# Kernel optimization log

Measured on AMD Instinct MI355X. Metric: run time of the kernel, lower is better.

Reference implementation:

```python
import jax, jax.numpy as jnp
import numpy as np

N_NODES = 100000
IN_DIM = 64
EMB_DIM = 128
N_EDGES = 1600000
BN_EPS = 1e-5
GIN_EPS = 0.0  # train_eps=False, default eps=0


def setup_inputs() -> dict:
    key = jax.random.key(0)
    ks = jax.random.split(key, 10)
    x = jax.random.normal(ks[0], (N_NODES, IN_DIM), dtype=jnp.float32)
    edge_index = jax.random.randint(ks[1], (2, N_EDGES), 0, N_NODES, dtype=jnp.int64)
    edge_attr = jax.random.normal(ks[2], (N_EDGES, 4), dtype=jnp.float32)  # unused by module
    edge_weight = jax.random.uniform(ks[3], (N_EDGES,), dtype=jnp.float32)
    # MLP params: Linear(in,emb) -> BN(emb) -> ReLU -> Linear(emb,emb)
    lim1 = 1.0 / np.sqrt(IN_DIM)
    W1 = jax.random.uniform(ks[4], (IN_DIM, EMB_DIM), minval=-lim1, maxval=lim1, dtype=jnp.float32)
    b1 = jax.random.uniform(ks[5], (EMB_DIM,), minval=-lim1, maxval=lim1, dtype=jnp.float32)
    gamma = jnp.ones((EMB_DIM,), dtype=jnp.float32)
    beta = jnp.zeros((EMB_DIM,), dtype=jnp.float32)
    lim2 = 1.0 / np.sqrt(EMB_DIM)
    W2 = jax.random.uniform(ks[6], (EMB_DIM, EMB_DIM), minval=-lim2, maxval=lim2, dtype=jnp.float32)
    b2 = jax.random.uniform(ks[7], (EMB_DIM,), minval=-lim2, maxval=lim2, dtype=jnp.float32)
    return {"x": x, "edge_index": edge_index, "edge_attr": edge_attr,
            "edge_weight": edge_weight, "W1": W1, "b1": b1,
            "gamma": gamma, "beta": beta, "W2": W2, "b2": b2}


def reference(x, edge_index, edge_attr, edge_weight, W1, b1, gamma, beta, W2, b2):
    src, dst = edge_index[0], edge_index[1]  # message from x[src] aggregated at dst
    msg = x[src] * edge_weight[:, None]                       # [E, in_dim] gather + scale
    agg = jax.ops.segment_sum(msg, dst, num_segments=x.shape[0])  # [N, in_dim] scatter-add
    out = agg + (1.0 + GIN_EPS) * x                           # GIN self term
    # MLP: Linear -> BatchNorm1d (training stats, biased var) -> ReLU -> Linear
    h = out @ W1 + b1                                         # [N, emb]
    mean = jnp.mean(h, axis=0)
    var = jnp.var(h, axis=0)
    h = (h - mean) * jax.lax.rsqrt(var + BN_EPS) * gamma + beta
    h = jax.nn.relu(h)
    return h @ W2 + b2
```

## Files before the change

### kernel.cpp

```cpp
#include <hip/hip_runtime.h>

#define N_NODES 100000
#define IN_DIM 64
#define EMB 128
#define N_EDGES 1600000
#define BN_EPS 1e-5f

#define NB 98
#define BCAP 18432
#define FA_THREADS 512
#define FA_EPT 16
#define FA_BLK (FA_THREADS * FA_EPT)
#define FA_GRID ((N_EDGES + FA_BLK - 1) / FA_BLK)

#define WS_GSUM     0
#define WS_GSUM2    512
#define WS_BCUR     1024
#define WS_ROWSTART 2048
#define WS_PAIRS    802304
#define WS_AGG      13602304
#define WS_DSTARR   39202304
#define WS_SWARR    46427648
#define WS_X16      WS_DSTARR
#define WS_ZERO_INTS 512

typedef _Float16 half8_t __attribute__((ext_vector_type(8)));
typedef _Float16 half4_t __attribute__((ext_vector_type(4)));
typedef _Float16 half2_t __attribute__((ext_vector_type(2)));
typedef float floatx4 __attribute__((ext_vector_type(4)));

__global__ __launch_bounds__(512) void zero_kernel(int* __restrict__ p)
{
    p[threadIdx.x] = 0;
}

__global__ __launch_bounds__(512) void fillA_kernel(
    const int* __restrict__ ei, const float* __restrict__ ew,
    int* __restrict__ bcur, int* __restrict__ dstArr, float2* __restrict__ swArr)
{
    __shared__ int cnt[NB], base[NB];
    const int tid = threadIdx.x;
    if (tid < NB) cnt[tid] = 0;
    __syncthreads();
    const int e0 = blockIdx.x * FA_BLK;
    int pk[FA_EPT];
    #pragma unroll
    for (int i = 0; i < FA_EPT; ++i) {
        int e = e0 + i * FA_THREADS + tid;
        pk[i] = -1;
        if (e < N_EDGES) {
            int d = ei[N_EDGES + e];
            int b = d >> 10;
            int pos = atomicAdd(&cnt[b], 1);
            pk[i] = (b << 13) | pos;
        }
    }
    __syncthreads();
    if (tid < NB) base[tid] = atomicAdd(&bcur[tid], cnt[tid]);
    __syncthreads();
    #pragma unroll
    for (int i = 0; i < FA_EPT; ++i) {
        int e = e0 + i * FA_THREADS + tid;
        if (pk[i] >= 0) {
            int b = pk[i] >> 13, pos = pk[i] & 8191;
            int idx = b * BCAP + base[b] + pos;
            dstArr[idx] = ei[N_EDGES + e];
            swArr[idx]  = make_float2(__int_as_float(ei[e]), ew[e]);
        }
    }
}

__global__ __launch_bounds__(1024) void fillB2_kernel(
    const int* __restrict__ bcur, const int* __restrict__ dstArr,
    const float2* __restrict__ swArr,
    int* __restrict__ rowstart, float2* __restrict__ pairs)
{
    __shared__ int cnt2[1024];
    __shared__ int pre[1024];
    __shared__ int sbk[128];
    const int g = blockIdx.x;
    const int tid = threadIdx.x;

    if (tid < 128) sbk[tid] = (tid < NB) ? bcur[tid] : 0;
    cnt2[tid] = 0;
    __syncthreads();
    for (int off = 1; off < 128; off <<= 1) {
        int v = 0;
        if (tid < 128 && tid >= off) v = sbk[tid - off];
        __syncthreads();
        if (tid < 128) sbk[tid] += v;
        __syncthreads();
    }
    const int bucketBase = (g > 0) ? sbk[g - 1] : 0;

    const int nE = bcur[g];
    const int segBase = g * BCAP;
    for (int j = tid; j < nE; j += 1024)
        atomicAdd(&cnt2[dstArr[segBase + j] & 1023], 1);
    __syncthreads();

    const int c = cnt2[tid];
    pre[tid] = c;
    __syncthreads();
    for (int off = 1; off < 1024; off <<= 1) {
        int v = (tid >= off) ? pre[tid - off] : 0;
        __syncthreads();
        pre[tid] += v;
        __syncthreads();
    }
    const int start = bucketBase + pre[tid] - c;
    const int node = g * 1024 + tid;
    if (node < N_NODES) rowstart[node] = start;
    if (node == N_NODES - 1) rowstart[N_NODES] = start + c;

    __syncthreads();
    cnt2[tid] = start;
    __syncthreads();
    #pragma unroll 4
    for (int j = tid; j < nE; j += 1024) {
        int d = dstArr[segBase + j];
        int p = atomicAdd(&cnt2[d & 1023], 1);
        pairs[p] = swArr[segBase + j];
    }
}

__global__ __launch_bounds__(256) void cvt_kernel(
    const float4* __restrict__ x4, ushort4* __restrict__ x16)
{
    int i = blockIdx.x * 256 + threadIdx.x;
    if (i >= N_NODES * IN_DIM / 4) return;
    float4 v = x4[i];
    ushort4 u;
    _Float16 a = (_Float16)v.x, b = (_Float16)v.y,
             c = (_Float16)v.z, d = (_Float16)v.w;
    u.x = *(unsigned short*)&a; u.y = *(unsigned short*)&b;
    u.z = *(unsigned short*)&c; u.w = *(unsigned short*)&d;
    x16[i] = u;
}

#define G_NPW 5
__global__ __launch_bounds__(256) void gather_kernel(
    const _Float16* __restrict__ x16,
    const int* __restrict__ rowstart,
    const float2* __restrict__ pairs,
    float* __restrict__ agg)
{
    const int tid  = threadIdx.x;
    const int lane = tid & 63;
    const int wid  = tid >> 6;
    const int e    = lane >> 4;
    const int f    = lane & 15;
    const half4_t* __restrict__ xv4 = (const half4_t*)x16;
    const int node0 = (blockIdx.x * 4 + wid) * G_NPW;

    for (int r = 0; r < G_NPW; ++r) {
        const int n  = node0 + r;
        const int jb = rowstart[n];
        const int je = rowstart[n + 1];
        float4 accA = make_float4(0.f, 0.f, 0.f, 0.f);
        float4 accB = make_float4(0.f, 0.f, 0.f, 0.f);
        for (int j0 = jb; j0 < je; j0 += 64) {
            const int cnt = min(64, je - j0);
            float2 p = (lane < cnt) ? pairs[j0 + lane] : make_float2(0.f, 0.f);
            int   psrc = __float_as_int(p.x);
            float pw   = p.y;
            const int nch = (cnt + 7) >> 3;
            #pragma unroll 4
            for (int c = 0; c < nch; ++c) {
                int   uA = __shfl(psrc, c * 8 + e);
                float wA = __shfl(pw,   c * 8 + e);
                int   uB = __shfl(psrc, c * 8 + 4 + e);
                float wB = __shfl(pw,   c * 8 + 4 + e);
                half4_t va = xv4[(size_t)(unsigned)uA * 16 + f];
                half4_t vb = xv4[(size_t)(unsigned)uB * 16 + f];
                accA.x += wA * (float)va[0]; accA.y += wA * (float)va[1];
                accA.z += wA * (float)va[2]; accA.w += wA * (float)va[3];
                accB.x += wB * (float)vb[0]; accB.y += wB * (float)vb[1];
                accB.z += wB * (float)vb[2]; accB.w += wB * (float)vb[3];
            }
        }
        float4 s = make_float4(accA.x + accB.x, accA.y + accB.y,
                               accA.z + accB.z, accA.w + accB.w);
        s.x += __shfl_xor(s.x, 16); s.y += __shfl_xor(s.y, 16);
        s.z += __shfl_xor(s.z, 16); s.w += __shfl_xor(s.w, 16);
        s.x += __shfl_xor(s.x, 32); s.y += __shfl_xor(s.y, 32);
        s.z += __shfl_xor(s.z, 32); s.w += __shfl_xor(s.w, 32);
        if (e == 0)
            *(float4*)&agg[(size_t)n * IN_DIM + f * 4] = s;
    }
}

#define GV_TPW 3
#define GV_TILES (N_NODES / 16)
#define GV_GRID ((GV_TILES + 4 * GV_TPW - 1) / (4 * GV_TPW))
__global__ __launch_bounds__(256) void gemv_kernel(
    const float* __restrict__ agg,
    const float* __restrict__ x,
    const float* __restrict__ W1,
    const float* __restrict__ b1,
    _Float16* __restrict__ h16,
    float* __restrict__ gsum, float* __restrict__ gsum2)
{
    __shared__ _Float16 w1t[EMB][72];
    __shared__ float redS[4][EMB], redQ[4][EMB];

    const int tid  = threadIdx.x;
    const int lane = tid & 63;
    const int wid  = tid >> 6;
    const int l15  = lane & 15;
    const int kb   = lane >> 4;

    #pragma unroll
    for (int i = 0; i < 32; ++i) {
        int idx = i * 256 + tid;
        int k = idx >> 7, c = idx & 127;
        w1t[c][k] = (_Float16)W1[idx];
    }
    float b1c[8];
    #pragma unroll
    for (int ct = 0; ct < 8; ++ct) b1c[ct] = b1[ct * 16 + l15];
    __syncthreads();

    half8_t Bf[8][2];
    #pragma unroll
    for (int ct = 0; ct < 8; ++ct)
        #pragma unroll
        for (int kc = 0; kc < 2; ++kc)
            Bf[ct][kc] = *(half8_t*)&w1t[ct * 16 + l15][kc * 32 + kb * 8];

    float sA[8] = {0,0,0,0,0,0,0,0};
    float qA[8] = {0,0,0,0,0,0,0,0};

    #pragma unroll
    for (int j = 0; j < GV_TPW; ++j) {
        const int t = blockIdx.x * (4 * GV_TPW) + wid * GV_TPW + j;
        if (t >= GV_TILES) break;
        const size_t rowb = (size_t)(t * 16 + l15) * IN_DIM + kb * 8;
        half8_t af[2];
        #pragma unroll
        for (int kc = 0; kc < 2; ++kc) {
            float4 a0 = *(const float4*)(agg + rowb + kc * 32);
            float4 a1 = *(const float4*)(agg + rowb + kc * 32 + 4);
            float4 x0 = *(const float4*)(x   + rowb + kc * 32);
            float4 x1 = *(const float4*)(x   + rowb + kc * 32 + 4);
            af[kc][0] = (_Float16)(a0.x + x0.x);
            af[kc][1] = (_Float16)(a0.y + x0.y);
            af[kc][2] = (_Float16)(a0.z + x0.z);
            af[kc][3] = (_Float16)(a0.w + x0.w);
            af[kc][4] = (_Float16)(a1.x + x1.x);
            af[kc][5] = (_Float16)(a1.y + x1.y);
            af[kc][6] = (_Float16)(a1.z + x1.z);
            af[kc][7] = (_Float16)(a1.w + x1.w);
        }
        floatx4 acc[8];
        #pragma unroll
        for (int ct = 0; ct < 8; ++ct)
            acc[ct] = (floatx4){b1c[ct], b1c[ct], b1c[ct], b1c[ct]};
        #pragma unroll
        for (int kc = 0; kc < 2; ++kc)
            #pragma unroll
            for (int ct = 0; ct < 8; ++ct)
                acc[ct] = __builtin_amdgcn_mfma_f32_16x16x32_f16(af[kc], Bf[ct][kc], acc[ct], 0, 0, 0);
        #pragma unroll
        for (int ct = 0; ct < 8; ++ct) {
            #pragma unroll
            for (int i = 0; i < 4; ++i) {
                const int r = t * 16 + kb * 4 + i;
                const float v = acc[ct][i];
                h16[(size_t)r * EMB + ct * 16 + l15] = (_Float16)v;
                sA[ct] += v;
                qA[ct] += v * v;
            }
        }
    }

    #pragma unroll
    for (int ct = 0; ct < 8; ++ct) {
        sA[ct] += __shfl_xor(sA[ct], 16); sA[ct] += __shfl_xor(sA[ct], 32);
        qA[ct] += __shfl_xor(qA[ct], 16); qA[ct] += __shfl_xor(qA[ct], 32);
    }
    if (lane < 16) {
        #pragma unroll
        for (int ct = 0; ct < 8; ++ct) {
            redS[wid][ct * 16 + lane] = sA[ct];
            redQ[wid][ct * 16 + lane] = qA[ct];
        }
    }
    __syncthreads();
    if (tid < EMB) {
        float s = redS[0][tid] + redS[1][tid] + redS[2][tid] + redS[3][tid];
        float q = redQ[0][tid] + redQ[1][tid] + redQ[2][tid] + redQ[3][tid];
        atomicAdd(&gsum[tid],  s);
        atomicAdd(&gsum2[tid], q);
    }
}

#define MR 32
#define M2_ITERS 5
#define M2_ROWS (MR * M2_ITERS)

__global__ __launch_bounds__(256) void mlp2_kernel(
    const _Float16* __restrict__ h16,
    float* __restrict__ out,
    const float* __restrict__ gsum, const float* __restrict__ gsum2,
    const float* __restrict__ gamma, const float* __restrict__ beta,
    const float* __restrict__ W2,
    const float* __restrict__ b2)
{
    __shared__ _Float16 Ph[MR][136];
    __shared__ float abuf[EMB], bbuf[EMB];

    const int tid  = threadIdx.x;
    const int lane = tid & 63;
    const int wid  = tid >> 6;
    const int rg   = wid >> 1;
    const int ch   = wid & 1;
    const int c0w  = ch * 64;
    const int l15  = lane & 15;
    const int kb   = lane >> 4;

    if (tid < EMB) {
        const float invN = 1.0f / (float)N_NODES;
        float mean = gsum[tid] * invN;
        float var  = gsum2[tid] * invN - mean * mean;
        float inv  = rsqrtf(var + BN_EPS);
        float a    = gamma[tid] * inv;
        abuf[tid] = a;
        bbuf[tid] = beta[tid] - mean * a;
    }

    const int bcol = c0w + l15;
    half8_t Bf[4][4];
    #pragma unroll
    for (int ct = 0; ct < 4; ++ct) {
        #pragma unroll
        for (int kc = 0; kc < 4; ++kc) {
            #pragma unroll
            for (int i = 0; i < 8; ++i)
                Bf[ct][kc][i] = (_Float16)W2[(kc * 32 + kb * 8 + i) * EMB + ct * 16 + bcol];
        }
    }
    float b2c[4];
    #pragma unroll
    for (int ct = 0; ct < 4; ++ct) b2c[ct] = b2[ct * 16 + bcol];

    __syncthreads();

    const int r0blk = blockIdx.x * M2_ROWS;
    for (int it = 0; it < M2_ITERS; ++it) {
        const int r0 = r0blk + it * MR;
        #pragma unroll
        for (int i = 0; i < 8; ++i) {
            int j   = i * 256 + tid;
            int row = j >> 6;
            int c2  = (j & 63) * 2;
            half2_t hv = *(const half2_t*)&h16[(size_t)(r0 + row) * EMB + c2];
            float p0 = fmaxf((float)hv[0] * abuf[c2]     + bbuf[c2],     0.f);
            float p1 = fmaxf((float)hv[1] * abuf[c2 + 1] + bbuf[c2 + 1], 0.f);
            Ph[row][c2]     = (_Float16)p0;
            Ph[row][c2 + 1] = (_Float16)p1;
        }
        __syncthreads();

        floatx4 acc[4];
        #pragma unroll
        for (int ct = 0; ct < 4; ++ct)
            acc[ct] = (floatx4){b2c[ct], b2c[ct], b2c[ct], b2c[ct]};
        #pragma unroll
        for (int kc = 0; kc < 4; ++kc) {
            half8_t af = *(half8_t*)&Ph[rg * 16 + l15][kc * 32 + kb * 8];
            #pragma unroll
            for (int ct = 0; ct < 4; ++ct)
                acc[ct] = __builtin_amdgcn_mfma_f32_16x16x32_f16(af, Bf[ct][kc], acc[ct], 0, 0, 0);
        }
        __syncthreads();

        #pragma unroll
        for (int ct = 0; ct < 4; ++ct) {
            #pragma unroll
            for (int i = 0; i < 4; ++i) {
                int row = r0 + rg * 16 + kb * 4 + i;
                out[(size_t)row * EMB + c0w + ct * 16 + l15] = acc[ct][i];
            }
        }
    }
}

extern "C" void kernel_launch(void* const* d_in, const int* in_sizes, int n_in,
                              void* d_out, int out_size, void* d_ws, size_t ws_size,
                              hipStream_t stream)
{
    const float* x     = (const float*)d_in[0];
    const int*   ei    = (const int*)d_in[1];
    const float* ew    = (const float*)d_in[3];
    const float* W1    = (const float*)d_in[4];
    const float* b1    = (const float*)d_in[5];
    const float* gamma = (const float*)d_in[6];
    const float* beta  = (const float*)d_in[7];
    const float* W2    = (const float*)d_in[8];
    const float* b2    = (const float*)d_in[9];

    char* ws = (char*)d_ws;
    float*    gsum     = (float*)(ws + WS_GSUM);
    float*    gsum2    = (float*)(ws + WS_GSUM2);
    int*      bcur     = (int*)(ws + WS_BCUR);
    int*      rowstart = (int*)(ws + WS_ROWSTART);
    float2*   pairs    = (float2*)(ws + WS_PAIRS);
    float*    agg      = (float*)(ws + WS_AGG);
    _Float16* h16      = (_Float16*)(ws + WS_AGG);
    int*      dstArr   = (int*)(ws + WS_DSTARR);
    float2*   swArr    = (float2*)(ws + WS_SWARR);
    _Float16* x16      = (_Float16*)(ws + WS_X16);
    float*    out      = (float*)d_out;

    zero_kernel<<<1, WS_ZERO_INTS, 0, stream>>>((int*)d_ws);
    fillA_kernel<<<FA_GRID, FA_THREADS, 0, stream>>>(ei, ew, bcur, dstArr, swArr);
    fillB2_kernel<<<NB, 1024, 0, stream>>>(bcur, dstArr, swArr, rowstart, pairs);
    cvt_kernel<<<(N_NODES * IN_DIM / 4 + 255) / 256, 256, 0, stream>>>(
        (const float4*)x, (ushort4*)x16);
    gather_kernel<<<N_NODES / (4 * G_NPW), 256, 0, stream>>>(x16, rowstart, pairs, agg);
    gemv_kernel<<<GV_GRID, 256, 0, stream>>>(agg, x, W1, b1, h16, gsum, gsum2);
    mlp2_kernel<<<N_NODES / M2_ROWS, 256, 0, stream>>>(h16, out, gsum, gsum2, gamma, beta, W2, b2);
}
```

Measured before the change: 156.6 us.

## Fuse neighbor gather with first linear layer and BN statistics

Merges the gather/aggregate kernel and the first MFMA GEMM kernel into one. Each block aggregates 32 nodes into a shared-memory fp16 tile, adding the self term from the fp16 copy of x, then runs the 64x128 product and BN partial sums from that tile. This removes the fp32 agg round trip through global memory and one launch. In exchange, every block reloads and converts W1 into shared memory, and the self term now uses fp16 x instead of fp32 x.

```diff
diff --git a/kernel.cpp b/kernel.cpp
--- a/kernel.cpp
+++ b/kernel.cpp
@@ -18,7 +18,7 @@
 #define WS_BCUR     1024
 #define WS_ROWSTART 2048
 #define WS_PAIRS    802304
-#define WS_AGG      13602304
+#define WS_H16      13602304
 #define WS_DSTARR   39202304
 #define WS_SWARR    46427648
 #define WS_X16      WS_DSTARR
@@ -138,23 +138,43 @@
     x16[i] = u;
 }
 
-#define G_NPW 5
-__global__ __launch_bounds__(256) void gather_kernel(
+#define GG_NPW 8
+__global__ __launch_bounds__(256) void gath_gemv_kernel(
     const _Float16* __restrict__ x16,
     const int* __restrict__ rowstart,
     const float2* __restrict__ pairs,
-    float* __restrict__ agg)
-{
+    const float* __restrict__ W1,
+    const float* __restrict__ b1,
+    _Float16* __restrict__ h16,
+    float* __restrict__ gsum, float* __restrict__ gsum2)
+{
+    __shared__ _Float16 w1t[EMB][72];
+    __shared__ _Float16 Ah[32][72];
+    __shared__ float redS[4][EMB], redQ[4][EMB];
+
     const int tid  = threadIdx.x;
     const int lane = tid & 63;
     const int wid  = tid >> 6;
     const int e    = lane >> 4;
     const int f    = lane & 15;
+    const int l15  = lane & 15;
+    const int kb   = lane >> 4;
     const half4_t* __restrict__ xv4 = (const half4_t*)x16;
-    const int node0 = (blockIdx.x * 4 + wid) * G_NPW;
-
-    for (int r = 0; r < G_NPW; ++r) {
-        const int n  = node0 + r;
+    const int node0 = blockIdx.x * 32;
+
+    #pragma unroll
+    for (int i = 0; i < 2; ++i) {
+        ((float*)redS)[i * 256 + tid] = 0.f;
+        ((float*)redQ)[i * 256 + tid] = 0.f;
+    }
+    #pragma unroll
+    for (int i = 0; i < 32; ++i) {
+        int idx = i * 256 + tid;
+        w1t[idx & 127][idx >> 7] = (_Float16)W1[idx];
+    }
+
+    for (int r = 0; r < GG_NPW; ++r) {
+        const int n  = node0 + wid * GG_NPW + r;
         const int jb = rowstart[n];
         const int je = rowstart[n + 1];
         float4 accA = make_float4(0.f, 0.f, 0.f, 0.f);
@@ -185,105 +205,69 @@
         s.z += __shfl_xor(s.z, 16); s.w += __shfl_xor(s.w, 16);
         s.x += __shfl_xor(s.x, 32); s.y += __shfl_xor(s.y, 32);
         s.z += __shfl_xor(s.z, 32); s.w += __shfl_xor(s.w, 32);
-        if (e == 0)
-            *(float4*)&agg[(size_t)n * IN_DIM + f * 4] = s;
-    }
-}
-
-#define GV_TPW 3
-#define GV_TILES (N_NODES / 16)
-#define GV_GRID ((GV_TILES + 4 * GV_TPW - 1) / (4 * GV_TPW))
-__global__ __launch_bounds__(256) void gemv_kernel(
-    const float* __restrict__ agg,
-    const float* __restrict__ x,
-    const float* __restrict__ W1,
-    const float* __restrict__ b1,
-    _Float16* __restrict__ h16,
-    float* __restrict__ gsum, float* __restrict__ gsum2)
-{
-    __shared__ _Float16 w1t[EMB][72];
-    __shared__ float redS[4][EMB], redQ[4][EMB];
-
-    const int tid  = threadIdx.x;
-    const int lane = tid & 63;
-    const int wid  = tid >> 6;
-    const int l15  = lane & 15;
-    const int kb   = lane >> 4;
-
-    #pragma unroll
-    for (int i = 0; i < 32; ++i) {
-        int idx = i * 256 + tid;
-        int k = idx >> 7, c = idx & 127;
-        w1t[c][k] = (_Float16)W1[idx];
-    }
-    float b1c[8];
-    #pragma unroll
-    for (int ct = 0; ct < 8; ++ct) b1c[ct] = b1[ct * 16 + l15];
-    __syncthreads();
-
-    half8_t Bf[8][2];
-    #pragma unroll
-    for (int ct = 0; ct < 8; ++ct)
+        if (e == 0) {
+            half4_t sv = xv4[(size_t)n * 16 + f];
+            half4_t hrow;
+            hrow[0] = (_Float16)(s.x + (float)sv[0]);
+            hrow[1] = (_Float16)(s.y + (float)sv[1]);
+            hrow[2] = (_Float16)(s.z + (float)sv[2]);
+            hrow[3] = (_Float16)(s.w + (float)sv[3]);
+            *(half4_t*)&Ah[wid * GG_NPW + r][f * 4] = hrow;
+        }
+    }
+    __syncthreads();
+
+    const int rg  = wid >> 1;
+    const int ch  = wid & 1;
+    const int c0w = ch * 64;
+
+    half8_t Bf[4][2];
+    #pragma unroll
+    for (int ct = 0; ct < 4; ++ct)
         #pragma unroll
         for (int kc = 0; kc < 2; ++kc)
-            Bf[ct][kc] = *(half8_t*)&w1t[ct * 16 + l15][kc * 32 + kb * 8];
-
-    float sA[8] = {0,0,0,0,0,0,0,0};
-    float qA[8] = {0,0,0,0,0,0,0,0};
-
-    #pragma unroll
-    for (int j = 0; j < GV_TPW; ++j) {
-        const int t = blockIdx.x * (4 * GV_TPW) + wid * GV_TPW + j;
-        if (t >= GV_TILES) break;
-        const size_t rowb = (size_t)(t * 16 + l15) * IN_DIM + kb * 8;
-        half8_t af[2];
-        #pragma unroll
-        for (int kc = 0; kc < 2; ++kc) {
-            float4 a0 = *(const float4*)(agg + rowb + kc * 32);
-            float4 a1 = *(const float4*)(agg + rowb + kc * 32 + 4);
-            float4 x0 = *(const float4*)(x   + rowb + kc * 32);
-            float4 x1 = *(const float4*)(x   + rowb + kc * 32 + 4);
-            af[kc][0] = (_Float16)(a0.x + x0.x);
-            af[kc][1] = (_Float16)(a0.y + x0.y);
-            af[kc][2] = (_Float16)(a0.z + x0.z);
-            af[kc][3] = (_Float16)(a0.w + x0.w);
-            af[kc][4] = (_Float16)(a1.x + x1.x);
-            af[kc][5] = (_Float16)(a1.y + x1.y);
-            af[kc][6] = (_Float16)(a1.z + x1.z);
-            af[kc][7] = (_Float16)(a1.w + x1.w);
-        }
-        floatx4 acc[8];
-        #pragma unroll
-        for (int ct = 0; ct < 8; ++ct)
-            acc[ct] = (floatx4){b1c[ct], b1c[ct], b1c[ct], b1c[ct]};
-        #pragma unroll
-        for (int kc = 0; kc < 2; ++kc)
-            #pragma unroll
-            for (int ct = 0; ct < 8; ++ct)
-                acc[ct] = __builtin_amdgcn_mfma_f32_16x16x32_f16(af[kc], Bf[ct][kc], acc[ct], 0, 0, 0);
-        #pragma unroll
-        for (int ct = 0; ct < 8; ++ct) {
-            #pragma unroll
-            for (int i = 0; i < 4; ++i) {
-                const int r = t * 16 + kb * 4 + i;
-                const float v = acc[ct][i];
-                h16[(size_t)r * EMB + ct * 16 + l15] = (_Float16)v;
-                sA[ct] += v;
-                qA[ct] += v * v;
-            }
-        }
-    }
-
-    #pragma unroll
-    for (int ct = 0; ct < 8; ++ct) {
+            Bf[ct][kc] = *(half8_t*)&w1t[c0w + ct * 16 + l15][kc * 32 + kb * 8];
+    float b1c[4];
+    #pragma unroll
+    for (int ct = 0; ct < 4; ++ct) b1c[ct] = b1[c0w + ct * 16 + l15];
+
+    half8_t af[2];
+    #pragma unroll
+    for (int kc = 0; kc < 2; ++kc)
+        af[kc] = *(half8_t*)&Ah[rg * 16 + l15][kc * 32 + kb * 8];
+
+    floatx4 acc[4];
+    #pragma unroll
+    for (int ct = 0; ct < 4; ++ct)
+        acc[ct] = (floatx4){b1c[ct], b1c[ct], b1c[ct], b1c[ct]};
+    #pragma unroll
+    for (int kc = 0; kc < 2; ++kc)
+        #pragma unroll
+        for (int ct = 0; ct < 4; ++ct)
+            acc[ct] = __builtin_amdgcn_mfma_f32_16x16x32_f16(af[kc], Bf[ct][kc], acc[ct], 0, 0, 0);
+
+    float sA[4] = {0, 0, 0, 0}, qA[4] = {0, 0, 0, 0};
+    #pragma unroll
+    for (int ct = 0; ct < 4; ++ct) {
+        #pragma unroll
+        for (int i = 0; i < 4; ++i) {
+            const int r = node0 + rg * 16 + kb * 4 + i;
+            const float v = acc[ct][i];
+            h16[(size_t)r * EMB + c0w + ct * 16 + l15] = (_Float16)v;
+            sA[ct] += v;
+            qA[ct] += v * v;
+        }
+    }
+    #pragma unroll
+    for (int ct = 0; ct < 4; ++ct) {
         sA[ct] += __shfl_xor(sA[ct], 16); sA[ct] += __shfl_xor(sA[ct], 32);
         qA[ct] += __shfl_xor(qA[ct], 16); qA[ct] += __shfl_xor(qA[ct], 32);
     }
     if (lane < 16) {
         #pragma unroll
-        for (int ct = 0; ct < 8; ++ct) {
-            redS[wid][ct * 16 + lane] = sA[ct];
-            redQ[wid][ct * 16 + lane] = qA[ct];
+        for (int ct = 0; ct < 4; ++ct) {
+            redS[wid][c0w + ct * 16 + lane] = sA[ct];
+            redQ[wid][c0w + ct * 16 + lane] = qA[ct];
         }
     }
     __syncthreads();
@@ -406,8 +390,7 @@
     int*      bcur     = (int*)(ws + WS_BCUR);
     int*      rowstart = (int*)(ws + WS_ROWSTART);
     float2*   pairs    = (float2*)(ws + WS_PAIRS);
-    float*    agg      = (float*)(ws + WS_AGG);
-    _Float16* h16      = (_Float16*)(ws + WS_AGG);
+    _Float16* h16      = (_Float16*)(ws + WS_H16);
     int*      dstArr   = (int*)(ws + WS_DSTARR);
     float2*   swArr    = (float2*)(ws + WS_SWARR);
     _Float16* x16      = (_Float16*)(ws + WS_X16);
@@ -418,7 +401,7 @@
     fillB2_kernel<<<NB, 1024, 0, stream>>>(bcur, dstArr, swArr, rowstart, pairs);
     cvt_kernel<<<(N_NODES * IN_DIM / 4 + 255) / 256, 256, 0, stream>>>(
         (const float4*)x, (ushort4*)x16);
-    gather_kernel<<<N_NODES / (4 * G_NPW), 256, 0, stream>>>(x16, rowstart, pairs, agg);
-    gemv_kernel<<<GV_GRID, 256, 0, stream>>>(agg, x, W1, b1, h16, gsum, gsum2);
+    gath_gemv_kernel<<<N_NODES / 32, 256, 0, stream>>>(
+        x16, rowstart, pairs, W1, b1, h16, gsum, gsum2);
     mlp2_kernel<<<N_NODES / M2_ROWS, 256, 0, stream>>>(h16, out, gsum, gsum2, gamma, beta, W2, b2);
 }
```

After: 200.9 us. 28.3% more time.
